# Kernel optimization log

Hardware: AMD Instinct MI355X
Metric: run time of the kernel (lower is better)

Reference implementation:

```python
import jax, jax.numpy as jnp
import numpy as np
from itertools import combinations

A = 4          # anchor_points
K = 16         # neighbor_num
INTRA = A * (A - 1) // 2   # 6
CH = INTRA * 2 + A * A     # 28 = generator channels
B, N, S = 1, 8192, 4096
CIN, COUT = 64, 128


def cdist(x):
    # pairwise euclidean distances [B,N,N], zero-safe sqrt (zero grad at d=0)
    sq = jnp.sum(x * x, -1)
    d2 = sq[:, :, None] + sq[:, None, :] - 2.0 * jnp.einsum('bnc,bmc->bnm', x, x)
    d2 = jnp.maximum(d2, 0.0)
    m = d2 > 0
    return jnp.where(m, jnp.sqrt(jnp.where(m, d2, 1.0)), 0.0)


def index_points(points, idx):
    # points [B,N,...], idx [B,*] -> [B,*,...]
    return jax.vmap(lambda p, i: p[i])(points, idx)


def index_points_dists(dists, i1, i2):
    # dists [B,N,N]; result[b,...] = dists[b, i1[b,...], i2[b,...]]
    i1, i2 = jnp.broadcast_arrays(i1, i2)
    return jax.vmap(lambda d, a, b: d[a, b])(dists, i1, i2)


def generator(xyz):
    # RotationInvariantDistFea.forward(xyz, concat_raw_relative_fea=True)
    D = cdist(xyz)
    neg_nd, ni = jax.lax.top_k(-D, K)   # K >= A; smallest-K, sorted ascending
    nd = -neg_nd
    ai = ni[:, :, :A]
    # intra-anchor dists: dists to anchors 1..A-1 plus pairwise dists among them
    subs = [index_points_dists(D, ai[:, :, pi], ai[:, :, pj])[:, :, None]
            for pi, pj in combinations(range(1, A), 2)]
    intra = jnp.concatenate([nd[:, :, 1:A]] + subs, axis=2)  # [B,P,6]
    # inter-anchor dists: center anchors x neighbor anchors -> [B,P,K,A*A]
    nai = index_points(ai, ni)                                # [B,P,K,A]
    inter = index_points_dists(D, ai[:, :, None, :, None],
                               nai[:, :, :, None, :]).reshape(D.shape[0], D.shape[1], K, A * A)
    center = jnp.broadcast_to(intra[:, :, None, :], (intra.shape[0], intra.shape[1], K, INTRA))
    rf = jnp.concatenate([center, index_points(intra, ni), inter], axis=3)  # [B,P,K,28]
    return rf, ni, D


def mlp(x, W, b, g, be, act):
    # Linear + BatchNorm1d (training mode: stats over batch*points) + optional leaky_relu(0.2)
    y = x @ W + b
    mu = jnp.mean(y, (0, 1))
    var = jnp.var(y, (0, 1))
    y = (y - mu) * jax.lax.rsqrt(var + 1e-5) * g + be
    return jax.nn.leaky_relu(y, 0.2) if act else y


def forward(xyz, feature, sample_indexes, Ww, bw, gw, betaw, Wb, bb, gb, betab, Wo, bo, go, betao):
    rf_before, ni_before, D_before = generator(xyz)
    intra_before = rf_before[:, :, 0, :INTRA]
    xyz_s = index_points(xyz, sample_indexes)
    feat = index_points(feature, sample_indexes)
    intra_before = index_points(intra_before, sample_indexes)
    rf_after, ni_after, _ = generator(xyz_s)
    intra_after = rf_after[:, :, 0, :INTRA]
    a_before = index_points(ni_before[:, :, :A], sample_indexes)                  # [B,S,A]
    a_after = jax.vmap(lambda s, a: s[a])(sample_indexes, ni_after[:, :, :A])     # map to global idx
    inter = index_points_dists(D_before, a_before[:, :, :, None],
                               a_after[:, :, None, :]).reshape(B, S, A * A)
    adf = jnp.concatenate([intra_before, intra_after, inter], axis=2)             # [B,S,28]
    w = mlp(adf, Ww, bw, gw, betaw, False)
    bia = mlp(adf, Wb, bb, gb, betab, False)
    feat = jax.nn.leaky_relu(feat * w + bia, 0.2)
    feat = jnp.concatenate([feat, adf], axis=2)                                   # [B,S,92]
    feat = mlp(feat, Wo, bo, go, betao, True)                                     # [B,S,128]
    return xyz_s, feat, rf_after, ni_after


def setup_inputs():
    key = jax.random.key(0)
    ks = jax.random.split(key, 8)
    xyz = jax.random.normal(ks[0], (B, N, 3), jnp.float32)
    feature = jax.random.normal(ks[1], (B, N, CIN), jnp.float32)
    sample_indexes = jnp.stack([jax.random.permutation(jax.random.fold_in(ks[2], i), N)[:S]
                                for i in range(B)]).astype(jnp.int32)

    def lin(k, cin, cout):
        k1, k2 = jax.random.split(k)
        W = jax.random.normal(k1, (cin, cout), jnp.float32) / np.float32(np.sqrt(cin))
        b = jax.random.normal(k2, (cout,), jnp.float32) * 0.01
        return W, b, jnp.ones((cout,), jnp.float32), jnp.zeros((cout,), jnp.float32)

    Ww, bw, gw, betaw = lin(ks[5], CH, CIN)
    Wb, bb, gb, betab = lin(ks[6], CH, CIN)
    Wo, bo, go, betao = lin(ks[7], CH + CIN, COUT)
    return dict(xyz=xyz, feature=feature, sample_indexes=sample_indexes,
                Ww=Ww, bw=bw, gw=gw, betaw=betaw,
                Wb=Wb, bb=bb, gb=gb, betab=betab,
                Wo=Wo, bo=bo, go=go, betao=betao)


def reference(xyz, feature, sample_indexes, Ww, bw, gw, betaw, Wb, bb, gb, betab, Wo, bo, go, betao):
    return forward(xyz, feature, sample_indexes, Ww, bw, gw, betaw, Wb, bb, gb, betab, Wo, bo, go, betao)
```

## Files before the change

### kernel.cpp

```cpp
#include <hip/hip_runtime.h>
#include <hip/hip_bf16.h>
#include <math.h>

#define N_PTS 8192
#define S_PTS 4096
#define CAP 128
typedef unsigned long long u64;
typedef unsigned u32;

__device__ __forceinline__ float pair_dist_d(const float4 a, const float4 b) {
    double ax = a.x, ay = a.y, az = a.z;
    double bx = b.x, by = b.y, bz = b.z;
    double dx = ax - bx, dy = ay - by, dz = az - bz;
    double d2 = dx * dx + dy * dy + dz * dz;
    return d2 > 0.0 ? (float)sqrt(d2) : 0.0f;
}

__device__ __forceinline__ float d2_f32_gram(const float4 a, const float4 b) {
    float dot = __fadd_rn(__fadd_rn(__fmul_rn(a.x, b.x), __fmul_rn(a.y, b.y)),
                          __fmul_rn(a.z, b.z));
    float d2 = __fsub_rn(__fadd_rn(a.w, b.w), __fmul_rn(2.0f, dot));
    return fmaxf(d2, 0.0f);
}

__device__ __forceinline__ u32 bitonic64_u32(u32 v, int lane) {
#pragma unroll
    for (int k = 2; k <= 64; k <<= 1) {
#pragma unroll
        for (int j2 = k >> 1; j2 >= 1; j2 >>= 1) {
            u32 o = __shfl_xor(v, j2, 64);
            bool keepMin = (((lane & j2) == 0) == ((lane & k) == 0));
            bool less = o < v;
            v = keepMin ? (less ? o : v) : (less ? v : o);
        }
    }
    return v;
}

__device__ __forceinline__ u64 bitonic64_u64(u64 v, int lane) {
#pragma unroll
    for (int k = 2; k <= 64; k <<= 1) {
#pragma unroll
        for (int j2 = k >> 1; j2 >= 1; j2 >>= 1) {
            u64 o = __shfl_xor(v, j2, 64);
            bool keepMin = (((lane & j2) == 0) == ((lane & k) == 0));
            bool less = o < v;
            v = keepMin ? (less ? o : v) : (less ? v : o);
        }
    }
    return v;
}

__global__ __launch_bounds__(256) void stage_kernel(
        const float* __restrict__ xyz, const int* __restrict__ sidx,
        float4* __restrict__ cb, float4* __restrict__ ca,
        int* __restrict__ inv, float* __restrict__ out_xyz_s) {
    int i = blockIdx.x * blockDim.x + threadIdx.x;
    if (i < N_PTS) {
        float x = xyz[i * 3 + 0], y = xyz[i * 3 + 1], z = xyz[i * 3 + 2];
        float sq = __fadd_rn(__fadd_rn(__fmul_rn(x, x), __fmul_rn(y, y)),
                             __fmul_rn(z, z));
        cb[i] = make_float4(x, y, z, sq);
    }
    if (i < S_PTS) {
        int si = sidx[i];
        float x = xyz[si * 3 + 0], y = xyz[si * 3 + 1], z = xyz[si * 3 + 2];
        float sq = __fadd_rn(__fadd_rn(__fmul_rn(x, x), __fmul_rn(y, y)),
                             __fmul_rn(z, z));
        ca[i] = make_float4(x, y, z, sq);
        inv[si] = i;
        out_xyz_s[i * 3 + 0] = x;
        out_xyz_s[i * 3 + 1] = y;
        out_xyz_s[i * 3 + 2] = z;
    }
}

template <int K, bool AFTER>
__device__ u64 cold_ladder(const float4 q, const float4* __restrict__ cb,
                           const int* __restrict__ inv, int lane) {
    u64 L[K];
#pragma unroll
    for (int j = 0; j < K; ++j) L[j] = ~0ull;
    for (int c = lane; c < N_PTS; c += 64) {
        int low = c;
        bool ok = true;
        if (AFTER) { int iv = inv[c]; ok = iv >= 0; low = iv; }
        if (!ok) continue;
        float d2 = d2_f32_gram(q, cb[c]);
        float D = d2 > 0.0f ? __fsqrt_rn(d2) : 0.0f;
        u64 key = ((u64)__float_as_uint(D) << 32) | (u64)(u32)low;
        if (key < L[K - 1]) {
#pragma unroll
            for (int j = K - 1; j >= 1; --j)
                L[j] = (key < L[j - 1]) ? L[j - 1] : ((key < L[j]) ? key : L[j]);
            L[0] = (key < L[0]) ? key : L[0];
        }
    }
    u64 res = ~0ull;
#pragma unroll
    for (int r = 0; r < K; ++r) {
        u64 m = L[0];
#pragma unroll
        for (int off = 32; off >= 1; off >>= 1) {
            u64 o = __shfl_xor(m, off, 64);
            m = (o < m) ? o : m;
        }
        if (lane == r) res = m;
        if (L[0] == m) {
#pragma unroll
            for (int j = 0; j < K - 1; ++j) L[j] = L[j + 1];
            L[K - 1] = ~0ull;
        }
    }
    return res;
}

template <int K>
__device__ u64 finalize_sort(const u64* buf, u32 cnt, int lane) {
    if (cnt <= 64u) {
        u64 v = (lane < (int)cnt) ? buf[lane] : ~0ull;
        return bitonic64_u64(v, lane);
    }
    u64 L0 = ~0ull, L1 = ~0ull, L2 = ~0ull, L3 = ~0ull;
    for (u32 mm = lane; mm < cnt; mm += 64) {
        u64 kk = buf[mm];
        if (kk < L3) {
            if (kk < L1) {
                L3 = L2; L2 = L1;
                if (kk < L0) { L1 = L0; L0 = kk; } else L1 = kk;
            } else {
                if (kk < L2) { L3 = L2; L2 = kk; } else L3 = kk;
            }
        }
    }
    u64 res = ~0ull;
#pragma unroll
    for (int r = 0; r < K; ++r) {
        u64 mr = L0;
#pragma unroll
        for (int off = 32; off >= 1; off >>= 1) {
            u64 o = __shfl_xor(mr, off, 64);
            mr = (o < mr) ? o : mr;
        }
        if (lane == r) res = mr;
        if (L0 == mr) { L0 = L1; L1 = L2; L2 = L3; L3 = ~0ull; }
    }
    return res;
}

__global__ __launch_bounds__(256) void knn_kernel(
        const float4* __restrict__ cb, const float4* __restrict__ ca,
        const int* __restrict__ inv, const int* __restrict__ sidx,
        int* __restrict__ a_before, float* __restrict__ intra_before,
        int* __restrict__ ni_i, float* __restrict__ intra_after,
        float* __restrict__ out_ni) {
    __shared__ u32 smin[16][256];
    __shared__ u64 sbuf[16][CAP];
    __shared__ u32 staus[16];
    __shared__ u32 scnt[16];
    __shared__ float4 sq[8];
    int t = threadIdx.x, lane = t & 63, wid = t >> 6;
    int s0 = blockIdx.x * 8;
    if (t < 8) sq[t] = cb[sidx[s0 + t]];
    if (t < 16) scnt[t] = 0;
    __syncthreads();
    float4 q[8];
#pragma unroll
    for (int i = 0; i < 8; ++i) q[i] = sq[i];

    u32 mB[8], mA[8];
#pragma unroll
    for (int i = 0; i < 8; ++i) { mB[i] = ~0u; mA[i] = ~0u; }
    for (int c = t; c < N_PTS; c += 256) {
        float4 p = cb[c];
        bool smp = inv[c] >= 0;
#pragma unroll
        for (int i = 0; i < 8; ++i) {
            u32 b = __float_as_uint(d2_f32_gram(q[i], p));
            mB[i] = b < mB[i] ? b : mB[i];
            if (smp) mA[i] = b < mA[i] ? b : mA[i];
        }
    }
#pragma unroll
    for (int i = 0; i < 8; ++i) { smin[i][t] = mB[i]; smin[8 + i][t] = mA[i]; }
    __syncthreads();
#pragma unroll
    for (int m = 0; m < 4; ++m) {
        int st = wid * 4 + m;
        u32 v = smin[st][lane];
        u32 v2 = smin[st][lane + 64];  v = v2 < v ? v2 : v;
        v2 = smin[st][lane + 128];     v = v2 < v ? v2 : v;
        v2 = smin[st][lane + 192];     v = v2 < v ? v2 : v;
        v = bitonic64_u32(v, lane);
        int kk = (st < 8) ? 3 : 15;
        if (lane == kk) staus[st] = v;
    }
    __syncthreads();
    u32 tB[8], tA[8];
#pragma unroll
    for (int i = 0; i < 8; ++i) { tB[i] = staus[i]; tA[i] = staus[8 + i]; }

    for (int c = t; c < N_PTS; c += 256) {
        float4 p = cb[c];
        int iv = inv[c];
        bool smp = iv >= 0;
#pragma unroll
        for (int i = 0; i < 8; ++i) {
            u32 b = __float_as_uint(d2_f32_gram(q[i], p));
            bool qb = b <= tB[i];
            bool qa = smp && (b <= tA[i]);
            if (qb || qa) {
                float d2v = __uint_as_float(b);
                float D = d2v > 0.0f ? __fsqrt_rn(d2v) : 0.0f;
                u64 hk = (u64)__float_as_uint(D) << 32;
                if (qb) {
                    u32 pos = atomicAdd(&scnt[i], 1u);
                    if (pos < CAP) sbuf[i][pos] = hk | (u64)(u32)c;
                }
                if (qa) {
                    u32 pos = atomicAdd(&scnt[8 + i], 1u);
                    if (pos < CAP) sbuf[8 + i][pos] = hk | (u64)(u32)iv;
                }
            }
        }
    }
    __syncthreads();
#pragma unroll
    for (int m = 0; m < 4; ++m) {
        int st = wid * 4 + m;
        u32 cnt = scnt[st];
        if (st < 8) {
            int s = s0 + st;
            float4 qq = q[st];
            u64 res = (cnt <= CAP) ? finalize_sort<4>(sbuf[st], cnt, lane)
                                   : cold_ladder<4, false>(qq, cb, inv, lane);
            int idx = (int)(res & 0xffffffffull);
            if (lane < 4) a_before[s * 4 + lane] = idx;
            if (lane >= 1 && lane < 4)
                intra_before[s * 6 + (lane - 1)] = pair_dist_d(qq, cb[idx]);
            int i1 = __shfl(idx, 1, 64);
            int i2 = __shfl(idx, 2, 64);
            int i3 = __shfl(idx, 3, 64);
            if (lane < 3) {
                int pa = (lane == 2) ? i2 : i1;
                int pb = (lane == 0) ? i2 : i3;
                intra_before[s * 6 + 3 + lane] = pair_dist_d(cb[pa], cb[pb]);
            }
        } else {
            int s = s0 + (st - 8);
            float4 qq = q[st - 8];
            u64 res = (cnt <= CAP) ? finalize_sort<16>(sbuf[st], cnt, lane)
                                   : cold_ladder<16, true>(qq, cb, inv, lane);
            int idx = (int)(res & 0xffffffffull);
            if (lane < 16) {
                ni_i[s * 16 + lane] = idx;
                out_ni[s * 16 + lane] = (float)idx;
            }
            if (lane >= 1 && lane < 4)
                intra_after[s * 6 + (lane - 1)] = pair_dist_d(qq, ca[idx]);
            int i1 = __shfl(idx, 1, 64);
            int i2 = __shfl(idx, 2, 64);
            int i3 = __shfl(idx, 3, 64);
            if (lane < 3) {
                int pa = (lane == 2) ? i2 : i1;
                int pb = (lane == 0) ? i2 : i3;
                intra_after[s * 6 + 3 + lane] = pair_dist_d(ca[pa], ca[pb]);
            }
        }
    }
}

__global__ __launch_bounds__(256) void assemble_kernel(
        const float4* __restrict__ ca, const float4* __restrict__ cb,
        const int* __restrict__ ni_i, const float* __restrict__ intra_after,
        const int* __restrict__ a_before, const float* __restrict__ intra_before,
        const int* __restrict__ sidx,
        float* __restrict__ out_rf, float* __restrict__ adf) {
    __shared__ int s_ni[4][16];
    __shared__ float s_rf[4][16 * 28];
    __shared__ float s_ia[4][8];
    int t = threadIdx.x, wid = t >> 6, lane = t & 63;
    int s = blockIdx.x * 4 + wid;
    if (lane < 16) s_ni[wid][lane] = ni_i[s * 16 + lane];
    if (lane < 6) s_ia[wid][lane] = intra_after[s * 6 + lane];
    __syncthreads();

    int k = lane >> 2, qq = lane & 3;
    int nai_q = ni_i[s_ni[wid][k] * 16 + qq];
    float4 pq = ca[nai_q];
#pragma unroll
    for (int p = 0; p < 4; ++p) {
        float4 pp = ca[s_ni[wid][p]];
        s_rf[wid][k * 28 + 12 + p * 4 + qq] = pair_dist_d(pp, pq);
    }
    for (int idx = lane; idx < 16 * 12; idx += 64) {
        int kk = idx / 12, c = idx % 12;
        float v = (c < 6) ? s_ia[wid][c] : intra_after[s_ni[wid][kk] * 6 + (c - 6)];
        s_rf[wid][kk * 28 + c] = v;
    }
    if (lane < 16) {
        int p = lane >> 2, q2 = lane & 3;
        int ib = a_before[s * 4 + p];
        int ia = sidx[s_ni[wid][q2]];
        adf[s * 28 + 12 + lane] = pair_dist_d(cb[ib], cb[ia]);
    } else if (lane >= 32 && lane < 38) {
        adf[s * 28 + (lane - 32)] = intra_before[s * 6 + (lane - 32)];
    } else if (lane >= 40 && lane < 46) {
        adf[s * 28 + 6 + (lane - 40)] = s_ia[wid][lane - 40];
    }
    __syncthreads();
    const int base = s * 16 * 28;
    for (int idx = lane; idx < 16 * 28; idx += 64) out_rf[base + idx] = s_rf[wid][idx];
}

__global__ __launch_bounds__(256) void mlp1_kernel(
        const float* __restrict__ adf,
        const float* __restrict__ Ww, const float* __restrict__ bw,
        const float* __restrict__ Wb, const float* __restrict__ bb,
        float* __restrict__ y_wb) {
    __shared__ float sW[28 * 128];
    __shared__ float sb[128];
    __shared__ float sA[32 * 28];
    int t = threadIdx.x;
    for (int i = t; i < 28 * 128; i += 256) {
        int k = i >> 7, c = i & 127;
        sW[i] = (c < 64) ? Ww[k * 64 + c] : Wb[k * 64 + (c - 64)];
    }
    if (t < 128) sb[t] = (t < 64) ? bw[t] : bb[t - 64];
    int s0 = blockIdx.x * 32;
    for (int i = t; i < 32 * 28; i += 256) sA[i] = adf[s0 * 28 + i];
    __syncthreads();
    int sl = t >> 3, grp = t & 7;
    int s = s0 + sl;
    float acc[16];
#pragma unroll
    for (int k = 0; k < 16; ++k) acc[k] = sb[grp * 16 + k];
    for (int k2 = 0; k2 < 28; ++k2) {
        float a = sA[sl * 28 + k2];
#pragma unroll
        for (int k = 0; k < 16; ++k)
            acc[k] = fmaf(a, sW[k2 * 128 + grp * 16 + k], acc[k]);
    }
#pragma unroll
    for (int k = 0; k < 16; ++k) y_wb[(grp * 16 + k) * 4096 + s] = acc[k];
}

__global__ __launch_bounds__(256) void stats_kernel(
        const float* __restrict__ y,
        const float* __restrict__ g0, const float* __restrict__ be0,
        const float* __restrict__ g1, const float* __restrict__ be1, int csplit,
        float* __restrict__ scale, float* __restrict__ shift) {
    int c = blockIdx.x;
    const float* p = y + c * 4096;
    float s1 = 0.0f, s2 = 0.0f;
    for (int i = threadIdx.x; i < 4096; i += 256) {
        float v = p[i];
        s1 += v;
        s2 = fmaf(v, v, s2);
    }
    __shared__ float l1[256], l2[256];
    l1[threadIdx.x] = s1;
    l2[threadIdx.x] = s2;
    __syncthreads();
    for (int off = 128; off; off >>= 1) {
        if (threadIdx.x < off) {
            l1[threadIdx.x] += l1[threadIdx.x + off];
            l2[threadIdx.x] += l2[threadIdx.x + off];
        }
        __syncthreads();
    }
    if (threadIdx.x == 0) {
        float mean = l1[0] * (1.0f / 4096.0f);
        float var = l2[0] * (1.0f / 4096.0f) - mean * mean;
        float g = (c < csplit) ? g0[c] : g1[c - csplit];
        float be = (c < csplit) ? be0[c] : be1[c - csplit];
        float sc = g / sqrtf(var + 1e-5f);
        scale[c] = sc;
        shift[c] = be - mean * sc;
    }
}

__global__ __launch_bounds__(256) void mlp2_kernel(
        const float* __restrict__ y_wb,
        const float* __restrict__ scale1, const float* __restrict__ shift1,
        const float* __restrict__ feature, const int* __restrict__ sidx,
        const float* __restrict__ adf,
        const float* __restrict__ Wo, const float* __restrict__ bo,
        float* __restrict__ y_o) {
    __shared__ float sW[92 * 128];
    __shared__ float t2[16 * 129];
    __shared__ float scat[16 * 92];
    int t = threadIdx.x;
    int s0 = blockIdx.x * 16;
    for (int i = t; i < 92 * 128; i += 256) sW[i] = Wo[i];
    for (int i = t; i < 16 * 128; i += 256) {
        int row = i & 15, c = i >> 4;
        t2[row * 129 + c] = fmaf(y_wb[c * 4096 + s0 + row], scale1[c], shift1[c]);
    }
    __syncthreads();
    for (int rr = 0; rr < 16; rr += 4) {
        int r = rr + (t >> 6);
        int c = t & 63;
        int si = sidx[s0 + r];
        float f = feature[si * 64 + c];
        float v = fmaf(f, t2[r * 129 + c], t2[r * 129 + 64 + c]);
        scat[r * 92 + c] = v >= 0.0f ? v : 0.2f * v;
    }
    for (int i = t; i < 16 * 28; i += 256) {
        int row = i / 28, k = i % 28;
        scat[row * 92 + 64 + k] = adf[(s0 + row) * 28 + k];
    }
    __syncthreads();
    int r = t >> 4, cg = t & 15;
    float acc[8];
#pragma unroll
    for (int j = 0; j < 8; ++j) acc[j] = bo[cg * 8 + j];
    for (int c = 0; c < 92; ++c) {
        float a = scat[r * 92 + c];
#pragma unroll
        for (int j = 0; j < 8; ++j)
            acc[j] = fmaf(a, sW[c * 128 + cg * 8 + j], acc[j]);
    }
    int s = s0 + r;
#pragma unroll
    for (int j = 0; j < 8; ++j) y_o[(cg * 8 + j) * 4096 + s] = acc[j];
}

__global__ __launch_bounds__(256) void final_kernel(
        const float* __restrict__ y_o,
        const float* __restrict__ scale, const float* __restrict__ shift,
        float* __restrict__ out_feat) {
    int tid = blockIdx.x * 256 + threadIdx.x;
    int j = tid >> 12;
    int s = tid & 4095;
    float v = fmaf(y_o[tid], scale[j], shift[j]);
    v = v >= 0.0f ? v : 0.2f * v;
    out_feat[s * 128 + j] = v;
}

extern "C" void kernel_launch(void* const* d_in, const int* in_sizes, int n_in,
                              void* d_out, int out_size, void* d_ws, size_t ws_size,
                              hipStream_t stream) {
    const float* xyz = (const float*)d_in[0];
    const float* feature = (const float*)d_in[1];
    const int* sidx = (const int*)d_in[2];
    const float* Ww = (const float*)d_in[3];
    const float* bw = (const float*)d_in[4];
    const float* gw = (const float*)d_in[5];
    const float* betaw = (const float*)d_in[6];
    const float* Wb = (const float*)d_in[7];
    const float* bb = (const float*)d_in[8];
    const float* gb = (const float*)d_in[9];
    const float* betab = (const float*)d_in[10];
    const float* Wo = (const float*)d_in[11];
    const float* bo = (const float*)d_in[12];
    const float* go = (const float*)d_in[13];
    const float* betao = (const float*)d_in[14];

    float* out = (float*)d_out;
    float* out_xyz = out;
    float* out_feat = out + 12288;
    float* out_rf = out + 12288 + 524288;
    float* out_ni = out + 12288 + 524288 + 1835008;

    float* ws = (float*)d_ws;
    float4* cb = (float4*)ws;
    float4* ca = (float4*)(ws + 32768);
    int* a_before = (int*)(ws + 49152);
    float* intra_before = ws + 65536;
    int* ni_i = (int*)(ws + 90112);
    float* intra_after = ws + 155648;
    float* adf = ws + 180224;
    float* y_wb = ws + 294912;
    float* y_o = ws + 819200;
    float* scale1 = ws + 1343488;
    float* shift1 = ws + 1343616;
    float* scale_o = ws + 1343744;
    float* shift_o = ws + 1343872;
    int* inv = (int*)(ws + 1344000);

    hipMemsetAsync(inv, 0xFF, N_PTS * sizeof(int), stream);
    stage_kernel<<<32, 256, 0, stream>>>(xyz, sidx, cb, ca, inv, out_xyz);
    knn_kernel<<<512, 256, 0, stream>>>(cb, ca, inv, sidx, a_before, intra_before,
                                        ni_i, intra_after, out_ni);
    assemble_kernel<<<1024, 256, 0, stream>>>(ca, cb, ni_i, intra_after, a_before,
                                              intra_before, sidx, out_rf, adf);
    mlp1_kernel<<<128, 256, 0, stream>>>(adf, Ww, bw, Wb, bb, y_wb);
    stats_kernel<<<128, 256, 0, stream>>>(y_wb, gw, betaw, gb, betab, 64, scale1, shift1);
    mlp2_kernel<<<256, 256, 0, stream>>>(y_wb, scale1, shift1, feature, sidx, adf, Wo, bo, y_o);
    stats_kernel<<<128, 256, 0, stream>>>(y_o, go, betao, go, betao, 128, scale_o, shift_o);
    final_kernel<<<2048, 256, 0, stream>>>(y_o, scale_o, shift_o, out_feat);
}
```

Measured before the change: 189.6 us.

## Scan sampled points directly in KNN, halve block work, vectorize MLP weight loads

The KNN kernel now computes the after-sampling neighbor set by scanning the compact sampled-point array ca instead of masking the full cloud through an inverse index. This removes the memset, the inv scatter and the inv loads. Each block handles 4 queries instead of 8, so twice as many blocks run, and the overflow fallback becomes a repeated-scan top-k instead of a register ladder. The MLP kernels read weights with float4 loads, and mlp1 uses 16 samples per block over 256 blocks; the change trades reuse of each loaded point across queries for more parallelism and less redundant work.

```diff
diff --git a/kernel.cpp b/kernel.cpp
--- a/kernel.cpp
+++ b/kernel.cpp
@@ -4,7 +4,7 @@
 
 #define N_PTS 8192
 #define S_PTS 4096
-#define CAP 128
+#define CAP 256
 typedef unsigned long long u64;
 typedef unsigned u32;
 
@@ -54,7 +54,7 @@
 __global__ __launch_bounds__(256) void stage_kernel(
         const float* __restrict__ xyz, const int* __restrict__ sidx,
         float4* __restrict__ cb, float4* __restrict__ ca,
-        int* __restrict__ inv, float* __restrict__ out_xyz_s) {
+        float* __restrict__ out_xyz_s) {
     int i = blockIdx.x * blockDim.x + threadIdx.x;
     if (i < N_PTS) {
         float x = xyz[i * 3 + 0], y = xyz[i * 3 + 1], z = xyz[i * 3 + 2];
@@ -68,49 +68,33 @@
         float sq = __fadd_rn(__fadd_rn(__fmul_rn(x, x), __fmul_rn(y, y)),
                              __fmul_rn(z, z));
         ca[i] = make_float4(x, y, z, sq);
-        inv[si] = i;
         out_xyz_s[i * 3 + 0] = x;
         out_xyz_s[i * 3 + 1] = y;
         out_xyz_s[i * 3 + 2] = z;
     }
 }
 
-template <int K, bool AFTER>
-__device__ u64 cold_ladder(const float4 q, const float4* __restrict__ cb,
-                           const int* __restrict__ inv, int lane) {
-    u64 L[K];
-#pragma unroll
-    for (int j = 0; j < K; ++j) L[j] = ~0ull;
-    for (int c = lane; c < N_PTS; c += 64) {
-        int low = c;
-        bool ok = true;
-        if (AFTER) { int iv = inv[c]; ok = iv >= 0; low = iv; }
-        if (!ok) continue;
-        float d2 = d2_f32_gram(q, cb[c]);
-        float D = d2 > 0.0f ? __fsqrt_rn(d2) : 0.0f;
-        u64 key = ((u64)__float_as_uint(D) << 32) | (u64)(u32)low;
-        if (key < L[K - 1]) {
-#pragma unroll
-            for (int j = K - 1; j >= 1; --j)
-                L[j] = (key < L[j - 1]) ? L[j - 1] : ((key < L[j]) ? key : L[j]);
-            L[0] = (key < L[0]) ? key : L[0];
-        }
-    }
+template <int K>
+__device__ u64 rescan_topk(const float4 q, const float4* __restrict__ pts,
+                           int n, int lane) {
     u64 res = ~0ull;
-#pragma unroll
+    u64 prev = 0;
     for (int r = 0; r < K; ++r) {
-        u64 m = L[0];
+        u64 best = ~0ull;
+        for (int c = lane; c < n; c += 64) {
+            float d2 = d2_f32_gram(q, pts[c]);
+            float D = d2 > 0.0f ? __fsqrt_rn(d2) : 0.0f;
+            u64 key = ((u64)__float_as_uint(D) << 32) | (u64)(u32)c;
+            bool ok = (r == 0) || (key > prev);
+            if (ok && key < best) best = key;
+        }
 #pragma unroll
         for (int off = 32; off >= 1; off >>= 1) {
-            u64 o = __shfl_xor(m, off, 64);
-            m = (o < m) ? o : m;
-        }
-        if (lane == r) res = m;
-        if (L[0] == m) {
-#pragma unroll
-            for (int j = 0; j < K - 1; ++j) L[j] = L[j + 1];
-            L[K - 1] = ~0ull;
-        }
+            u64 o = __shfl_xor(best, off, 64);
+            best = (o < best) ? o : best;
+        }
+        if (lane == r) res = best;
+        prev = best;
     }
     return res;
 }
@@ -150,122 +134,126 @@
 
 __global__ __launch_bounds__(256) void knn_kernel(
         const float4* __restrict__ cb, const float4* __restrict__ ca,
-        const int* __restrict__ inv, const int* __restrict__ sidx,
+        const int* __restrict__ sidx,
         int* __restrict__ a_before, float* __restrict__ intra_before,
         int* __restrict__ ni_i, float* __restrict__ intra_after,
         float* __restrict__ out_ni) {
-    __shared__ u32 smin[16][256];
-    __shared__ u64 sbuf[16][CAP];
-    __shared__ u32 staus[16];
-    __shared__ u32 scnt[16];
-    __shared__ float4 sq[8];
+    __shared__ u32 smin[8][256];
+    __shared__ u64 sbuf[8][CAP];
+    __shared__ u32 staus[8];
+    __shared__ u32 scnt[8];
+    __shared__ float4 sq[4];
     int t = threadIdx.x, lane = t & 63, wid = t >> 6;
-    int s0 = blockIdx.x * 8;
-    if (t < 8) sq[t] = cb[sidx[s0 + t]];
-    if (t < 16) scnt[t] = 0;
-    __syncthreads();
-    float4 q[8];
-#pragma unroll
-    for (int i = 0; i < 8; ++i) q[i] = sq[i];
-
-    u32 mB[8], mA[8];
-#pragma unroll
-    for (int i = 0; i < 8; ++i) { mB[i] = ~0u; mA[i] = ~0u; }
+    int s0 = blockIdx.x * 4;
+    if (t < 4) sq[t] = cb[sidx[s0 + t]];
+    if (t < 8) scnt[t] = 0;
+    __syncthreads();
+    float4 q[4];
+#pragma unroll
+    for (int i = 0; i < 4; ++i) q[i] = sq[i];
+
+    u32 mB[4], mA[4];
+#pragma unroll
+    for (int i = 0; i < 4; ++i) { mB[i] = ~0u; mA[i] = ~0u; }
     for (int c = t; c < N_PTS; c += 256) {
         float4 p = cb[c];
-        bool smp = inv[c] >= 0;
-#pragma unroll
-        for (int i = 0; i < 8; ++i) {
+#pragma unroll
+        for (int i = 0; i < 4; ++i) {
             u32 b = __float_as_uint(d2_f32_gram(q[i], p));
             mB[i] = b < mB[i] ? b : mB[i];
-            if (smp) mA[i] = b < mA[i] ? b : mA[i];
-        }
-    }
-#pragma unroll
-    for (int i = 0; i < 8; ++i) { smin[i][t] = mB[i]; smin[8 + i][t] = mA[i]; }
-    __syncthreads();
-#pragma unroll
-    for (int m = 0; m < 4; ++m) {
-        int st = wid * 4 + m;
+        }
+    }
+    for (int c = t; c < S_PTS; c += 256) {
+        float4 p = ca[c];
+#pragma unroll
+        for (int i = 0; i < 4; ++i) {
+            u32 b = __float_as_uint(d2_f32_gram(q[i], p));
+            mA[i] = b < mA[i] ? b : mA[i];
+        }
+    }
+#pragma unroll
+    for (int i = 0; i < 4; ++i) { smin[i][t] = mB[i]; smin[4 + i][t] = mA[i]; }
+    __syncthreads();
+#pragma unroll
+    for (int m = 0; m < 2; ++m) {
+        int st = (m == 0) ? wid : wid + 4;
         u32 v = smin[st][lane];
         u32 v2 = smin[st][lane + 64];  v = v2 < v ? v2 : v;
         v2 = smin[st][lane + 128];     v = v2 < v ? v2 : v;
         v2 = smin[st][lane + 192];     v = v2 < v ? v2 : v;
         v = bitonic64_u32(v, lane);
-        int kk = (st < 8) ? 3 : 15;
+        int kk = (st < 4) ? 3 : 15;
         if (lane == kk) staus[st] = v;
     }
     __syncthreads();
-    u32 tB[8], tA[8];
-#pragma unroll
-    for (int i = 0; i < 8; ++i) { tB[i] = staus[i]; tA[i] = staus[8 + i]; }
+    u32 tB[4], tA[4];
+#pragma unroll
+    for (int i = 0; i < 4; ++i) { tB[i] = staus[i]; tA[i] = staus[4 + i]; }
 
     for (int c = t; c < N_PTS; c += 256) {
         float4 p = cb[c];
-        int iv = inv[c];
-        bool smp = iv >= 0;
-#pragma unroll
-        for (int i = 0; i < 8; ++i) {
+#pragma unroll
+        for (int i = 0; i < 4; ++i) {
             u32 b = __float_as_uint(d2_f32_gram(q[i], p));
-            bool qb = b <= tB[i];
-            bool qa = smp && (b <= tA[i]);
-            if (qb || qa) {
+            if (b <= tB[i]) {
                 float d2v = __uint_as_float(b);
                 float D = d2v > 0.0f ? __fsqrt_rn(d2v) : 0.0f;
-                u64 hk = (u64)__float_as_uint(D) << 32;
-                if (qb) {
-                    u32 pos = atomicAdd(&scnt[i], 1u);
-                    if (pos < CAP) sbuf[i][pos] = hk | (u64)(u32)c;
-                }
-                if (qa) {
-                    u32 pos = atomicAdd(&scnt[8 + i], 1u);
-                    if (pos < CAP) sbuf[8 + i][pos] = hk | (u64)(u32)iv;
-                }
+                u32 pos = atomicAdd(&scnt[i], 1u);
+                if (pos < CAP)
+                    sbuf[i][pos] = ((u64)__float_as_uint(D) << 32) | (u64)(u32)c;
             }
         }
     }
-    __syncthreads();
-#pragma unroll
-    for (int m = 0; m < 4; ++m) {
-        int st = wid * 4 + m;
-        u32 cnt = scnt[st];
-        if (st < 8) {
-            int s = s0 + st;
-            float4 qq = q[st];
-            u64 res = (cnt <= CAP) ? finalize_sort<4>(sbuf[st], cnt, lane)
-                                   : cold_ladder<4, false>(qq, cb, inv, lane);
-            int idx = (int)(res & 0xffffffffull);
-            if (lane < 4) a_before[s * 4 + lane] = idx;
-            if (lane >= 1 && lane < 4)
-                intra_before[s * 6 + (lane - 1)] = pair_dist_d(qq, cb[idx]);
-            int i1 = __shfl(idx, 1, 64);
-            int i2 = __shfl(idx, 2, 64);
-            int i3 = __shfl(idx, 3, 64);
-            if (lane < 3) {
-                int pa = (lane == 2) ? i2 : i1;
-                int pb = (lane == 0) ? i2 : i3;
-                intra_before[s * 6 + 3 + lane] = pair_dist_d(cb[pa], cb[pb]);
+    for (int c = t; c < S_PTS; c += 256) {
+        float4 p = ca[c];
+#pragma unroll
+        for (int i = 0; i < 4; ++i) {
+            u32 b = __float_as_uint(d2_f32_gram(q[i], p));
+            if (b <= tA[i]) {
+                float d2v = __uint_as_float(b);
+                float D = d2v > 0.0f ? __fsqrt_rn(d2v) : 0.0f;
+                u32 pos = atomicAdd(&scnt[4 + i], 1u);
+                if (pos < CAP)
+                    sbuf[4 + i][pos] = ((u64)__float_as_uint(D) << 32) | (u64)(u32)c;
             }
-        } else {
-            int s = s0 + (st - 8);
-            float4 qq = q[st - 8];
-            u64 res = (cnt <= CAP) ? finalize_sort<16>(sbuf[st], cnt, lane)
-                                   : cold_ladder<16, true>(qq, cb, inv, lane);
-            int idx = (int)(res & 0xffffffffull);
-            if (lane < 16) {
-                ni_i[s * 16 + lane] = idx;
-                out_ni[s * 16 + lane] = (float)idx;
-            }
-            if (lane >= 1 && lane < 4)
-                intra_after[s * 6 + (lane - 1)] = pair_dist_d(qq, ca[idx]);
-            int i1 = __shfl(idx, 1, 64);
-            int i2 = __shfl(idx, 2, 64);
-            int i3 = __shfl(idx, 3, 64);
-            if (lane < 3) {
-                int pa = (lane == 2) ? i2 : i1;
-                int pb = (lane == 0) ? i2 : i3;
-                intra_after[s * 6 + 3 + lane] = pair_dist_d(ca[pa], ca[pb]);
-            }
+        }
+    }
+    __syncthreads();
+    {
+        int s = s0 + wid;
+        float4 qq = q[wid];
+        u32 cnt = scnt[wid];
+        u64 res = (cnt <= CAP) ? finalize_sort<4>(sbuf[wid], cnt, lane)
+                               : rescan_topk<4>(qq, cb, N_PTS, lane);
+        int idx = (int)(res & 0xffffffffull);
+        if (lane < 4) a_before[s * 4 + lane] = idx;
+        if (lane >= 1 && lane < 4)
+            intra_before[s * 6 + (lane - 1)] = pair_dist_d(qq, cb[idx]);
+        int i1 = __shfl(idx, 1, 64);
+        int i2 = __shfl(idx, 2, 64);
+        int i3 = __shfl(idx, 3, 64);
+        if (lane < 3) {
+            int pa = (lane == 2) ? i2 : i1;
+            int pb = (lane == 0) ? i2 : i3;
+            intra_before[s * 6 + 3 + lane] = pair_dist_d(cb[pa], cb[pb]);
+        }
+        cnt = scnt[4 + wid];
+        res = (cnt <= CAP) ? finalize_sort<16>(sbuf[4 + wid], cnt, lane)
+                           : rescan_topk<16>(qq, ca, S_PTS, lane);
+        idx = (int)(res & 0xffffffffull);
+        if (lane < 16) {
+            ni_i[s * 16 + lane] = idx;
+            out_ni[s * 16 + lane] = (float)idx;
+        }
+        if (lane >= 1 && lane < 4)
+            intra_after[s * 6 + (lane - 1)] = pair_dist_d(qq, ca[idx]);
+        i1 = __shfl(idx, 1, 64);
+        i2 = __shfl(idx, 2, 64);
+        i3 = __shfl(idx, 3, 64);
+        if (lane < 3) {
+            int pa = (lane == 2) ? i2 : i1;
+            int pb = (lane == 0) ? i2 : i3;
+            intra_after[s * 6 + 3 + lane] = pair_dist_d(ca[pa], ca[pb]);
         }
     }
 }
@@ -320,29 +308,36 @@
         float* __restrict__ y_wb) {
     __shared__ float sW[28 * 128];
     __shared__ float sb[128];
-    __shared__ float sA[32 * 28];
+    __shared__ float sA[16 * 28];
     int t = threadIdx.x;
     for (int i = t; i < 28 * 128; i += 256) {
         int k = i >> 7, c = i & 127;
         sW[i] = (c < 64) ? Ww[k * 64 + c] : Wb[k * 64 + (c - 64)];
     }
     if (t < 128) sb[t] = (t < 64) ? bw[t] : bb[t - 64];
-    int s0 = blockIdx.x * 32;
-    for (int i = t; i < 32 * 28; i += 256) sA[i] = adf[s0 * 28 + i];
-    __syncthreads();
-    int sl = t >> 3, grp = t & 7;
+    int s0 = blockIdx.x * 16;
+    for (int i = t; i < 16 * 28; i += 256) sA[i] = adf[s0 * 28 + i];
+    __syncthreads();
+    int sl = t >> 4, grp = t & 15;
     int s = s0 + sl;
-    float acc[16];
-#pragma unroll
-    for (int k = 0; k < 16; ++k) acc[k] = sb[grp * 16 + k];
+    float acc[8];
+#pragma unroll
+    for (int k = 0; k < 8; ++k) acc[k] = sb[grp * 8 + k];
     for (int k2 = 0; k2 < 28; ++k2) {
         float a = sA[sl * 28 + k2];
-#pragma unroll
-        for (int k = 0; k < 16; ++k)
-            acc[k] = fmaf(a, sW[k2 * 128 + grp * 16 + k], acc[k]);
-    }
-#pragma unroll
-    for (int k = 0; k < 16; ++k) y_wb[(grp * 16 + k) * 4096 + s] = acc[k];
+        float4 w0 = *(const float4*)&sW[k2 * 128 + grp * 8];
+        float4 w1 = *(const float4*)&sW[k2 * 128 + grp * 8 + 4];
+        acc[0] = fmaf(a, w0.x, acc[0]);
+        acc[1] = fmaf(a, w0.y, acc[1]);
+        acc[2] = fmaf(a, w0.z, acc[2]);
+        acc[3] = fmaf(a, w0.w, acc[3]);
+        acc[4] = fmaf(a, w1.x, acc[4]);
+        acc[5] = fmaf(a, w1.y, acc[5]);
+        acc[6] = fmaf(a, w1.z, acc[6]);
+        acc[7] = fmaf(a, w1.w, acc[7]);
+    }
+#pragma unroll
+    for (int k = 0; k < 8; ++k) y_wb[(grp * 8 + k) * 4096 + s] = acc[k];
 }
 
 __global__ __launch_bounds__(256) void stats_kernel(
@@ -417,9 +412,16 @@
     for (int j = 0; j < 8; ++j) acc[j] = bo[cg * 8 + j];
     for (int c = 0; c < 92; ++c) {
         float a = scat[r * 92 + c];
-#pragma unroll
-        for (int j = 0; j < 8; ++j)
-            acc[j] = fmaf(a, sW[c * 128 + cg * 8 + j], acc[j]);
+        float4 w0 = *(const float4*)&sW[c * 128 + cg * 8];
+        float4 w1 = *(const float4*)&sW[c * 128 + cg * 8 + 4];
+        acc[0] = fmaf(a, w0.x, acc[0]);
+        acc[1] = fmaf(a, w0.y, acc[1]);
+        acc[2] = fmaf(a, w0.z, acc[2]);
+        acc[3] = fmaf(a, w0.w, acc[3]);
+        acc[4] = fmaf(a, w1.x, acc[4]);
+        acc[5] = fmaf(a, w1.y, acc[5]);
+        acc[6] = fmaf(a, w1.z, acc[6]);
+        acc[7] = fmaf(a, w1.w, acc[7]);
     }
     int s = s0 + r;
 #pragma unroll
@@ -477,15 +479,13 @@
     float* shift1 = ws + 1343616;
     float* scale_o = ws + 1343744;
     float* shift_o = ws + 1343872;
-    int* inv = (int*)(ws + 1344000);
-
-    hipMemsetAsync(inv, 0xFF, N_PTS * sizeof(int), stream);
-    stage_kernel<<<32, 256, 0, stream>>>(xyz, sidx, cb, ca, inv, out_xyz);
-    knn_kernel<<<512, 256, 0, stream>>>(cb, ca, inv, sidx, a_before, intra_before,
-                                        ni_i, intra_after, out_ni);
+
+    stage_kernel<<<32, 256, 0, stream>>>(xyz, sidx, cb, ca, out_xyz);
+    knn_kernel<<<1024, 256, 0, stream>>>(cb, ca, sidx, a_before, intra_before,
+                                         ni_i, intra_after, out_ni);
     assemble_kernel<<<1024, 256, 0, stream>>>(ca, cb, ni_i, intra_after, a_before,
                                               intra_before, sidx, out_rf, adf);
-    mlp1_kernel<<<128, 256, 0, stream>>>(adf, Ww, bw, Wb, bb, y_wb);
+    mlp1_kernel<<<256, 256, 0, stream>>>(adf, Ww, bw, Wb, bb, y_wb);
     stats_kernel<<<128, 256, 0, stream>>>(y_wb, gw, betaw, gb, betab, 64, scale1, shift1);
     mlp2_kernel<<<256, 256, 0, stream>>>(y_wb, scale1, shift1, feature, sidx, adf, Wo, bo, y_o);
     stats_kernel<<<128, 256, 0, stream>>>(y_o, go, betao, go, betao, 128, scale_o, shift_o);
```

New measurement: 182.8 us. 1.04x faster.
